# Performance work log

Measured on AMD Instinct MI355X. Metric: run time of the kernel, lower is better.

The kernel has to match this reference:

```python
import jax, jax.numpy as jnp
import numpy as np


def setup_inputs() -> dict:
    key = jax.random.key(0)
    k1, k2 = jax.random.split(key)
    P, D = 2048, 256
    feat_q = jax.random.normal(k1, (P, D), dtype=jnp.float32)
    feat_k = jax.random.normal(k2, (P, D), dtype=jnp.float32)
    return {"feat_q": feat_q, "feat_k": feat_k}


def reference(feat_q, feat_k):
    # feat_k is detached in the original module
    feat_k = jax.lax.stop_gradient(feat_k)
    # per-patch rank-1 outer products: [P, D, D]
    d_q = feat_q[:, :, None] * feat_q[:, None, :]
    d_k = feat_k[:, :, None] * feat_k[:, None, :]
    # L1Loss default reduction = mean over all elements
    loss = jnp.mean(jnp.abs(d_q - d_k))
    return loss
```

## Files before the change

kernel.cpp:

```cpp
#include <hip/hip_runtime.h>
#include <hip/hip_bf16.h>


#define PATCHES 2048
#define DIM 256

__global__ __launch_bounds__(DIM) void patch_l1_partial(
    const float* __restrict__ q,
    const float* __restrict__ k,
    float* __restrict__ partial)
{
    __shared__ float qs[DIM];
    __shared__ float ks[DIM];

    const int p = blockIdx.x;
    const int t = threadIdx.x;

    const float* __restrict__ qrow = q + (size_t)p * DIM;
    const float* __restrict__ krow = k + (size_t)p * DIM;

    const float qi = qrow[t];
    const float ki = krow[t];
    qs[t] = qi;
    ks[t] = ki;
    __syncthreads();

    float acc = 0.0f;
#pragma unroll 8
    for (int j = 0; j < DIM; ++j) {
        const float v = qi * qs[j] - ki * ks[j];
        acc += fabsf(v);
    }

#pragma unroll
    for (int off = 32; off > 0; off >>= 1)
        acc += __shfl_down(acc, off, 64);

    __shared__ float wsum[4];
    const int wave = t >> 6;
    const int lane = t & 63;
    if (lane == 0) wsum[wave] = acc;
    __syncthreads();

    if (t == 0)
        partial[p] = (wsum[0] + wsum[1]) + (wsum[2] + wsum[3]);
}

__global__ __launch_bounds__(256) void patch_l1_final(
    const float* __restrict__ partial,
    float* __restrict__ out)
{
    const int t = threadIdx.x;
    float acc = 0.0f;
#pragma unroll
    for (int i = t; i < PATCHES; i += 256)
        acc += partial[i];

#pragma unroll
    for (int off = 32; off > 0; off >>= 1)
        acc += __shfl_down(acc, off, 64);

    __shared__ float wsum[4];
    if ((t & 63) == 0) wsum[t >> 6] = acc;
    __syncthreads();

    if (t == 0) {
        const float s = (wsum[0] + wsum[1]) + (wsum[2] + wsum[3]);
        const double denom = (double)PATCHES * (double)DIM * (double)DIM;
        out[0] = (float)((double)s / denom);
    }
}

extern "C" void kernel_launch(void* const* d_in, const int* in_sizes, int n_in,
                              void* d_out, int out_size, void* d_ws, size_t ws_size,
                              hipStream_t stream)
{
    const float* q = (const float*)d_in[0];
    const float* k = (const float*)d_in[1];
    float* out = (float*)d_out;
    float* partial = (float*)d_ws;

    patch_l1_partial<<<PATCHES, DIM, 0, stream>>>(q, k, partial);
    patch_l1_final<<<1, 256, 0, stream>>>(partial, out);
}
```

Measured before the change: 72.96 us.

## Assign one patch per wave with float4 register-blocked outer-product tiles

Each block now handles four patches, one per wave, and patches are loaded with float4 vector loads. Each lane holds 8 row elements in registers and sweeps half the columns with float4 LDS reads, using four independent accumulators. The per-block cross-wave reduction and its second barrier are gone. The aim is to cut LDS read traffic per FMA and shorten the dependency chain, at the cost of more registers per thread.

After: 70.42 us. -3.5%, faster.

```diff
diff --git a/kernel.cpp b/kernel.cpp
--- a/kernel.cpp
+++ b/kernel.cpp
@@ -4,46 +4,70 @@
 
 #define PATCHES 2048
 #define DIM 256
+#define PPB 4
 
-__global__ __launch_bounds__(DIM) void patch_l1_partial(
-    const float* __restrict__ q,
-    const float* __restrict__ k,
+__global__ __launch_bounds__(256) void patch_l1_partial(
+    const float4* __restrict__ q4,
+    const float4* __restrict__ k4,
     float* __restrict__ partial)
 {
-    __shared__ float qs[DIM];
-    __shared__ float ks[DIM];
+    __shared__ float4 qs[PPB][DIM / 4];
+    __shared__ float4 ks[PPB][DIM / 4];
 
-    const int p = blockIdx.x;
-    const int t = threadIdx.x;
+    const int t  = threadIdx.x;
+    const int p0 = blockIdx.x * PPB;
 
-    const float* __restrict__ qrow = q + (size_t)p * DIM;
-    const float* __restrict__ krow = k + (size_t)p * DIM;
-
-    const float qi = qrow[t];
-    const float ki = krow[t];
-    qs[t] = qi;
-    ks[t] = ki;
+    {
+        const int lp = t >> 6;
+        const int e  = t & 63;
+        qs[lp][e] = q4[(size_t)(p0 + lp) * (DIM / 4) + e];
+        ks[lp][e] = k4[(size_t)(p0 + lp) * (DIM / 4) + e];
+    }
     __syncthreads();
 
-    float acc = 0.0f;
-#pragma unroll 8
-    for (int j = 0; j < DIM; ++j) {
-        const float v = qi * qs[j] - ki * ks[j];
-        acc += fabsf(v);
+    const int wave = t >> 6;
+    const int lane = t & 63;
+    const int half = lane >> 5;
+    const int cg   = lane & 31;
+
+    const float4 qi0 = qs[wave][2 * cg];
+    const float4 qi1 = qs[wave][2 * cg + 1];
+    const float4 ki0 = ks[wave][2 * cg];
+    const float4 ki1 = ks[wave][2 * cg + 1];
+
+    const int jb0 = half * 32;
+
+    float a0 = 0.f, a1 = 0.f, a2 = 0.f, a3 = 0.f;
+
+#define ACC4(A, QV, KV, C)                              \
+    A += fabsf(QV.C * qj.x - KV.C * kj.x);              \
+    A += fabsf(QV.C * qj.y - KV.C * kj.y);              \
+    A += fabsf(QV.C * qj.z - KV.C * kj.z);              \
+    A += fabsf(QV.C * qj.w - KV.C * kj.w);
+
+#pragma unroll 4
+    for (int jb = 0; jb < 32; ++jb) {
+        const float4 qj = qs[wave][jb0 + jb];
+        const float4 kj = ks[wave][jb0 + jb];
+        ACC4(a0, qi0, ki0, x)
+        ACC4(a1, qi0, ki0, y)
+        ACC4(a2, qi0, ki0, z)
+        ACC4(a3, qi0, ki0, w)
+        ACC4(a0, qi1, ki1, x)
+        ACC4(a1, qi1, ki1, y)
+        ACC4(a2, qi1, ki1, z)
+        ACC4(a3, qi1, ki1, w)
     }
+#undef ACC4
+
+    float acc = (a0 + a1) + (a2 + a3);
 
 #pragma unroll
     for (int off = 32; off > 0; off >>= 1)
         acc += __shfl_down(acc, off, 64);
 
-    __shared__ float wsum[4];
-    const int wave = t >> 6;
-    const int lane = t & 63;
-    if (lane == 0) wsum[wave] = acc;
-    __syncthreads();
-
-    if (t == 0)
-        partial[p] = (wsum[0] + wsum[1]) + (wsum[2] + wsum[3]);
+    if (lane == 0)
+        partial[p0 + wave] = acc;
 }
 
 __global__ __launch_bounds__(256) void patch_l1_final(
@@ -75,11 +99,11 @@
                               void* d_out, int out_size, void* d_ws, size_t ws_size,
                               hipStream_t stream)
 {
-    const float* q = (const float*)d_in[0];
-    const float* k = (const float*)d_in[1];
+    const float4* q4 = (const float4*)d_in[0];
+    const float4* k4 = (const float4*)d_in[1];
     float* out = (float*)d_out;
     float* partial = (float*)d_ws;
 
-    patch_l1_partial<<<PATCHES, DIM, 0, stream>>>(q, k, partial);
+    patch_l1_partial<<<PATCHES / PPB, 256, 0, stream>>>(q4, k4, partial);
     patch_l1_final<<<1, 256, 0, stream>>>(partial, out);
 }
```
